# Performance work log

Measured on AMD Instinct MI355X. Metric: run time of the kernel, lower is better.

The kernel has to match this reference:

```python
import jax, jax.numpy as jnp
import numpy as np

H, IN, L, R = 128, 64, 3, 7
Nc, Na, Nx = 10000, 40000, 100000
NS = (Nc, Na, Nx)
ES = (50000, 100000, 100000, 150000, 200000, 200000, 200000)
# relation order: cc, c->a, a->c, aa, a->x, x->a, xx  (0=core,1=agg,2=access)
SRC_T = (0, 0, 1, 1, 1, 2, 2)
DST_T = (0, 1, 0, 1, 2, 1, 2)


def setup_inputs() -> dict:
    key = jax.random.key(0)
    ks = iter(jax.random.split(key, 80))
    d = {}
    for name, n in (("x_core", Nc), ("x_agg", Na), ("x_access", Nx)):
        d[name] = jax.random.normal(next(ks), (n, IN), jnp.float32)
    for r in range(R):
        d[f"src{r}"] = jax.random.randint(next(ks), (ES[r],), 0, NS[SRC_T[r]])
        d[f"dst{r}"] = jax.random.randint(next(ks), (ES[r],), 0, NS[DST_T[r]])
        d[f"ea{r}"] = jax.random.normal(next(ks), (ES[r], 3), jnp.float32)

    def w(k, shape, fan):
        return (jax.random.normal(k, shape, jnp.float32) / np.float32(np.sqrt(fan)))

    for nt in ("core", "agg", "access"):
        d[f"linW_{nt}"] = w(next(ks), (IN, H), IN)
        d[f"linb_{nt}"] = jnp.zeros((H,), jnp.float32)
    d["eW"] = w(next(ks), (L, R, 3, H), 3)       # GINEConv edge Linear(3->H)
    d["eb"] = jnp.zeros((L, R, H), jnp.float32)
    d["W1"] = w(next(ks), (L, R, H, H), H)        # MLP first Linear
    d["b1"] = jnp.zeros((L, R, H), jnp.float32)
    d["g1"] = jnp.ones((L, R, H), jnp.float32)    # BatchNorm gamma
    d["be1"] = jnp.zeros((L, R, H), jnp.float32)  # BatchNorm beta
    d["W2"] = w(next(ks), (L, R, H, H), H)        # MLP second Linear
    d["b2"] = jnp.zeros((L, R, H), jnp.float32)
    return d


def _forward(x_core, x_agg, x_access,
             linW_core, linb_core, linW_agg, linb_agg, linW_access, linb_access,
             eW, eb, W1, b1, g1, be1, W2, b2, srcs, dsts, eas):
    elu = jax.nn.elu
    h = [elu(x_core @ linW_core + linb_core),
         elu(x_agg @ linW_agg + linb_agg),
         elu(x_access @ linW_access + linb_access)]
    bn_inv = 1.0 / jnp.sqrt(jnp.float32(1.0 + 1e-5))  # eval BN: running mean 0, var 1
    for l in range(L):
        out = [jnp.zeros_like(ht) for ht in h]
        for r in range(R):
            s, t = SRC_T[r], DST_T[r]
            # GINEConv message: ReLU(x_j + Lin(edge_attr))  -> [E, H]
            msg = jax.nn.relu(h[s][srcs[r]] + eas[r] @ eW[l, r] + eb[l, r])
            agg = jax.ops.segment_sum(msg, dsts[r], num_segments=h[t].shape[0])
            z = h[t] + agg  # (1+eps)*x_i + aggr, eps=0
            # PyG MLP([H,H,H]): Linear -> BatchNorm -> ReLU -> Linear
            z = jax.nn.relu((z @ W1[l, r] + b1[l, r]) * bn_inv * g1[l, r] + be1[l, r])
            out[t] = out[t] + (z @ W2[l, r] + b2[l, r])  # HeteroConv aggr='sum'
        # residual + ELU; dropout is identity in eval mode
        h = [elu(out[t] + h[t]) for t in range(3)]
    return tuple(h)


def reference(x_core, x_agg, x_access,
              src0, dst0, ea0, src1, dst1, ea1, src2, dst2, ea2,
              src3, dst3, ea3, src4, dst4, ea4, src5, dst5, ea5,
              src6, dst6, ea6,
              linW_core, linb_core, linW_agg, linb_agg, linW_access, linb_access,
              eW, eb, W1, b1, g1, be1, W2, b2):
    srcs = (src0, src1, src2, src3, src4, src5, src6)
    dsts = (dst0, dst1, dst2, dst3, dst4, dst5, dst6)
    eas = (ea0, ea1, ea2, ea3, ea4, ea5, ea6)
    return _forward(x_core, x_agg, x_access,
                    linW_core, linb_core, linW_agg, linb_agg, linW_access, linb_access,
                    eW, eb, W1, b1, g1, be1, W2, b2, srcs, dsts, eas)
```

## Files before the change

kernel.cpp:

```cpp
#include <hip/hip_runtime.h>
#include <math.h>

#define H 128

typedef __attribute__((ext_vector_type(8))) short short8;
typedef __attribute__((ext_vector_type(4))) float f32x4;

static const int SRC_T_[7] = {0, 0, 1, 1, 1, 2, 2};
static const int DST_T_[7] = {0, 1, 0, 1, 2, 1, 2};

__device__ __forceinline__ float eluf(float x) {
    return x > 0.f ? x : (__expf(x) - 1.f);
}
__device__ __forceinline__ unsigned short f2bf(float x) {
    union { float f; unsigned int u; } v; v.f = x;
    unsigned int r = v.u + 0x7fffu + ((v.u >> 16) & 1u);
    return (unsigned short)(r >> 16);
}
__device__ __forceinline__ float bf2f(unsigned int u) {
    union { unsigned int u; float f; } v; v.u = u << 16;
    return v.f;
}

#define GLDS16(gp, lp) __builtin_amdgcn_global_load_lds( \
    (const __attribute__((address_space(1))) void*)(gp), \
    (__attribute__((address_space(3))) void*)(lp), 16, 0, 0)

struct PreCtx {
    const int* dst[7];
    int* deg;
    int E[7], bOff[8], hOff[8];
    const float* W1; const float* W2; const float* linW[3];
    unsigned short* wp; unsigned short* wlin;
    int gEnd;
};

__global__ __launch_bounds__(256) void k_pre(PreCtx P)
{
    const int b = blockIdx.x;
    const int tid = threadIdx.x;

    if (b < P.hOff[7]) {
        int r = 0;
        while (b >= P.hOff[r + 1]) ++r;
        const int lb = b - P.hOff[r];
        const int nb = P.hOff[r + 1] - P.hOff[r];
        const int* dst = P.dst[r];
        int* degr = P.deg + (P.bOff[r] << 8);
        for (int e = lb * 256 + tid; e < P.E[r]; e += nb * 256)
            atomicAdd(&degr[dst[e]], 1);
        return;
    }
    {
        const int lb = b - P.hOff[7];
        const int gw = P.gEnd - P.hOff[7];
        for (int i = lb * 256 + tid; i < 21 * 16384; i += gw * 256) {
            int lr = i >> 14, rem = i & 16383;
            int c = rem >> 7, k = rem & 127;
            P.wp[(size_t)(lr * 2 + 0) * 16384 + rem] = f2bf(P.W1[(size_t)lr * 16384 + k * H + c]);
            P.wp[(size_t)(lr * 2 + 1) * 16384 + rem] = f2bf(P.W2[(size_t)lr * 16384 + k * H + c]);
        }
        for (int i = lb * 256 + tid; i < 3 * 8192; i += gw * 256) {
            int t = i >> 13, rem = i & 8191;
            int c = rem >> 6, k = rem & 63;
            P.wlin[t * 8192 + c * 64 + k] = f2bf(P.linW[t][k * H + c]);
        }
    }
}

struct InCtx {
    const float* x[3]; const float* linb[3];
    unsigned short* hb[3]; int n[3];
    int gend[3];
};

__global__ __launch_bounds__(512, 2) void k_input_mfma(
    InCtx I, const unsigned short* __restrict__ wlin)
{
    __shared__ unsigned short xb[128 * 64];
    __shared__ unsigned short ob[128 * H];

    const int b = blockIdx.x;
    const int t = (b >= I.gend[0] ? 1 : 0) + (b >= I.gend[1] ? 1 : 0);
    const int lb = b - (t == 0 ? 0 : I.gend[t - 1]);
    const int n = I.n[t];
    const int tid = threadIdx.x;
    const int lane = tid & 63;
    const int wave = tid >> 6;
    const int wr = wave >> 2;
    const int wc = wave & 3;
    const int l15 = lane & 15;
    const int lq  = lane >> 4;
    const int c0 = wc * 32 + l15;
    const int r0 = lb * 128;
    const int rows = min(128, n - r0);
    const float* x = I.x[t];

    for (int idx = tid; idx < 128 * 16; idx += 512) {
        const int row = idx >> 4, cg = (idx & 15) << 2;
        uint2 p;
        if (row < rows) {
            f32x4 v = *(const f32x4*)&x[(size_t)(r0 + row) * 64 + cg];
            p.x = (unsigned int)f2bf(v.x) | ((unsigned int)f2bf(v.y) << 16);
            p.y = (unsigned int)f2bf(v.z) | ((unsigned int)f2bf(v.w) << 16);
        } else { p.x = 0; p.y = 0; }
        *(uint2*)&xb[row * 64 + (cg ^ ((row & 7) << 3))] = p;
    }
    const unsigned short* wt = wlin + (size_t)t * 8192;
    short8 wf[2][2];
#pragma unroll
    for (int nf = 0; nf < 2; ++nf)
#pragma unroll
        for (int kc = 0; kc < 2; ++kc)
            wf[nf][kc] = *(const short8*)&wt[(c0 + nf * 16) * 64 + kc * 32 + (lq << 3)];
    const float bc0 = I.linb[t][c0], bc1 = I.linb[t][c0 + 16];
    __syncthreads();

    const f32x4 Z4 = {0.f, 0.f, 0.f, 0.f};
    f32x4 acc[4][2];
#pragma unroll
    for (int rb = 0; rb < 4; ++rb)
#pragma unroll
        for (int nf = 0; nf < 2; ++nf) acc[rb][nf] = Z4;
#pragma unroll
    for (int kc = 0; kc < 2; ++kc) {
        const int kb = kc * 32 + (lq << 3);
        short8 af[4];
#pragma unroll
        for (int rb = 0; rb < 4; ++rb) {
            const int row = wr * 64 + rb * 16 + l15;
            af[rb] = *(const short8*)&xb[row * 64 + (kb ^ ((row & 7) << 3))];
        }
#pragma unroll
        for (int rb = 0; rb < 4; ++rb)
#pragma unroll
            for (int nf = 0; nf < 2; ++nf)
                acc[rb][nf] = __builtin_amdgcn_mfma_f32_16x16x32_bf16(
                    af[rb], wf[nf][kc], acc[rb][nf], 0, 0, 0);
    }
#pragma unroll
    for (int rb = 0; rb < 4; ++rb)
#pragma unroll
        for (int nf = 0; nf < 2; ++nf) {
            const int col = c0 + nf * 16;
            const float bc = nf == 0 ? bc0 : bc1;
#pragma unroll
            for (int rg = 0; rg < 4; ++rg) {
                const int row = wr * 64 + rb * 16 + (lq << 2) + rg;
                ob[row * H + col] = f2bf(eluf(acc[rb][nf][rg] + bc));
            }
        }
    __syncthreads();
    uint2* d = (uint2*)&I.hb[t][(size_t)r0 * H];
    const uint2* s2 = (const uint2*)ob;
    for (int idx = tid; idx < rows * 32; idx += 512) d[idx] = s2[idx];
}

struct CsrCtx {
    const int* src[7]; const int* dst[7]; const float* ea[7];
    int* csr_src[7]; uint2* csr_ea[7]; int* ptr[7];
    int* deg; int* cursor; int* bsum;
    int eOff[8];
    int bOff[8];
    int nd[7];
};

__global__ __launch_bounds__(256) void k_scan_partial_all(CsrCtx C)
{
    __shared__ int s[256];
    const int b = blockIdx.x;
    int r = 0;
    while (b >= C.bOff[r + 1]) ++r;
    const int lb = b - C.bOff[r];
    const int tid = threadIdx.x;
    const int idx = lb * 256 + tid;
    s[tid] = idx < C.nd[r] ? C.deg[(C.bOff[r] << 8) + idx] : 0;
    __syncthreads();
    for (int off = 128; off > 0; off >>= 1) {
        if (tid < off) s[tid] += s[tid + off];
        __syncthreads();
    }
    if (tid == 0) C.bsum[b] = s[0];
}

__global__ __launch_bounds__(512) void k_scan_mid_all(CsrCtx C)
{
    __shared__ int s[512];
    const int r = blockIdx.x;
    const int nb = C.bOff[r + 1] - C.bOff[r];
    const int tid = threadIdx.x;
    const int v = tid < nb ? C.bsum[C.bOff[r] + tid] : 0;
    s[tid] = v;
    __syncthreads();
    for (int off = 1; off < 512; off <<= 1) {
        int t = (tid >= off) ? s[tid - off] : 0;
        __syncthreads();
        s[tid] += t;
        __syncthreads();
    }
    if (tid < nb) C.bsum[C.bOff[r] + tid] = s[tid] - v;
    if (tid == nb - 1) C.ptr[r][C.nd[r]] = s[tid];
}

__global__ __launch_bounds__(256) void k_scan_final_all(CsrCtx C)
{
    __shared__ int s[256];
    const int b = blockIdx.x;
    int r = 0;
    while (b >= C.bOff[r + 1]) ++r;
    const int lb = b - C.bOff[r];
    const int tid = threadIdx.x;
    const int idx = lb * 256 + tid;
    const int v = idx < C.nd[r] ? C.deg[(C.bOff[r] << 8) + idx] : 0;
    s[tid] = v;
    __syncthreads();
    for (int off = 1; off < 256; off <<= 1) {
        int t = (tid >= off) ? s[tid - off] : 0;
        __syncthreads();
        s[tid] += t;
        __syncthreads();
    }
    if (idx < C.nd[r]) {
        const int excl = s[tid] - v + C.bsum[b];
        C.ptr[r][idx] = excl;
        C.cursor[(C.bOff[r] << 8) + idx] = excl;
    }
}

__global__ __launch_bounds__(256) void k_scatter_all(CsrCtx C, int Etot)
{
    for (int e = blockIdx.x * 256 + threadIdx.x; e < Etot; e += gridDim.x * 256) {
        int r = 0;
        while (e >= C.eOff[r + 1]) ++r;
        const int le = e - C.eOff[r];
        const int d = C.dst[r][le];
        const int pos = atomicAdd(&C.cursor[(C.bOff[r] << 8) + d], 1);
        C.csr_src[r][pos] = C.src[r][le];
        const float* eap = C.ea[r] + (size_t)3 * le;
        uint2 p;
        p.x = (unsigned int)f2bf(eap[0]) | ((unsigned int)f2bf(eap[1]) << 16);
        p.y = (unsigned int)f2bf(eap[2]);
        C.csr_ea[r][pos] = p;
    }
}

struct AggCtx {
    const int* ptr[7]; const int* csr_src[7]; const uint2* csr_ea[7];
    const unsigned short* hsrc[7]; const unsigned short* hdst[7];
    unsigned short* z[7];
    int gOff[8];
    int nd[7];
};

__global__ __launch_bounds__(256) void k_aggz_all(
    AggCtx A, const float* __restrict__ eW, const float* __restrict__ eb, int l)
{
    const int b = blockIdx.x;
    int r = 0;
    while (b >= A.gOff[r + 1]) ++r;
    const int lb = b - A.gOff[r];
    const int wave = threadIdx.x >> 6;
    const int lane = threadIdx.x & 63;
    const int t2 = lane << 1;
    const int lr = l * 7 + r;
    const float* eWr = eW + (size_t)lr * 3 * H;
    const float* ebr = eb + (size_t)lr * H;
    const float w00 = eWr[t2],         w01 = eWr[t2 + 1];
    const float w10 = eWr[H + t2],     w11 = eWr[H + t2 + 1];
    const float w20 = eWr[2 * H + t2], w21 = eWr[2 * H + t2 + 1];
    const float b0 = ebr[t2], b1v = ebr[t2 + 1];

    const int nd = A.nd[r];
    const int d0 = lb * 64 + wave * 16;
    if (d0 >= nd) return;
    const int dend = min(d0 + 16, nd);
    const int* __restrict__ ptr = A.ptr[r];
    const int* __restrict__ cs = A.csr_src[r];
    const uint2* __restrict__ ce = A.csr_ea[r];
    const unsigned short* __restrict__ hs = A.hsrc[r];
    const unsigned short* __restrict__ hd = A.hdst[r];
    unsigned int* __restrict__ zp = (unsigned int*)A.z[r];

    int pA = ptr[d0];
    int pB = ptr[d0 + 1];
    unsigned int hdvC = ((const unsigned int*)&hd[(size_t)d0 * H])[lane];

    for (int d = d0; d < dend; ++d) {
        int pNext = 0; unsigned int hdvN = 0;
        if (d + 1 < dend) {
            pNext = ptr[d + 2];
            hdvN = ((const unsigned int*)&hd[(size_t)(d + 1) * H])[lane];
        }
        float acc0 = bf2f(hdvC & 0xffffu);
        float acc1 = bf2f(hdvC >> 16);
        int i = pA;
        const int p1 = pB;
        if (i + 1 < p1) {
            int s0 = cs[i], s1 = cs[i + 1];
            uint2 eC0 = ce[i], eC1 = ce[i + 1];
            unsigned int hvC0 = ((const unsigned int*)&hs[(size_t)s0 * H])[lane];
            unsigned int hvC1 = ((const unsigned int*)&hs[(size_t)s1 * H])[lane];
            for (;;) {
                const int jn = i + 2;
                const bool more = (jn + 1 < p1);
                uint2 eN0, eN1; unsigned int hvN0 = 0, hvN1 = 0;
                if (more) {
                    const int sN0 = cs[jn], sN1 = cs[jn + 1];
                    eN0 = ce[jn]; eN1 = ce[jn + 1];
                    hvN0 = ((const unsigned int*)&hs[(size_t)sN0 * H])[lane];
                    hvN1 = ((const unsigned int*)&hs[(size_t)sN1 * H])[lane];
                }
                const float a00 = bf2f(eC0.x & 0xffffu), a01 = bf2f(eC0.x >> 16), a02 = bf2f(eC0.y & 0xffffu);
                const float a10 = bf2f(eC1.x & 0xffffu), a11 = bf2f(eC1.x >> 16), a12 = bf2f(eC1.y & 0xffffu);
                acc0 += fmaxf(bf2f(hvC0 & 0xffffu) + a00 * w00 + a01 * w10 + a02 * w20 + b0, 0.f)
                      + fmaxf(bf2f(hvC1 & 0xffffu) + a10 * w00 + a11 * w10 + a12 * w20 + b0, 0.f);
                acc1 += fmaxf(bf2f(hvC0 >> 16) + a00 * w01 + a01 * w11 + a02 * w21 + b1v, 0.f)
                      + fmaxf(bf2f(hvC1 >> 16) + a10 * w01 + a11 * w11 + a12 * w21 + b1v, 0.f);
                i = jn;
                if (!more) break;
                eC0 = eN0; eC1 = eN1; hvC0 = hvN0; hvC1 = hvN1;
            }
        }
        if (i < p1) {
            const int s = cs[i];
            const uint2 ep = ce[i];
            const float a0 = bf2f(ep.x & 0xffffu);
            const float a1 = bf2f(ep.x >> 16);
            const float a2 = bf2f(ep.y & 0xffffu);
            const unsigned int hv = ((const unsigned int*)&hs[(size_t)s * H])[lane];
            acc0 += fmaxf(bf2f(hv & 0xffffu) + a0 * w00 + a1 * w10 + a2 * w20 + b0, 0.f);
            acc1 += fmaxf(bf2f(hv >> 16)     + a0 * w01 + a1 * w11 + a2 * w21 + b1v, 0.f);
        }
        zp[(size_t)d * 64 + (lane ^ ((d & 7) << 2))] =
            (unsigned int)f2bf(acc0) | ((unsigned int)f2bf(acc1) << 16);
        pA = pB; pB = pNext; hdvC = hdvN;
    }
}

struct MlpCtx {
    const unsigned short* z[3][3];
    int lr[3][3];
    int nrel[3];
    int gend[3];
    int noffH[3];
    int n[3];
};

__global__ __launch_bounds__(512, 2) void k_mlp_all(
    MlpCtx M, const unsigned short* __restrict__ hb,
    unsigned short* __restrict__ hbw, float* __restrict__ fout,
    const unsigned short* __restrict__ wprep,
    const float* __restrict__ b1g, const float* __restrict__ g1g,
    const float* __restrict__ be1g, const float* __restrict__ b2g, int fin)
{
    __shared__ unsigned short smem[2 * 128 * H];
    unsigned short* zt  = smem;
    unsigned short* a1t = smem + 128 * H;

    const int b = blockIdx.x;
    const int t = (b >= M.gend[0] ? 1 : 0) + (b >= M.gend[1] ? 1 : 0);
    const int lb = b - (t == 0 ? 0 : M.gend[t - 1]);
    const int n = M.n[t];
    const int nrel = M.nrel[t];
    const unsigned short* hbp = hb + (size_t)M.noffH[t];

    const int tid = threadIdx.x;
    const int lane = tid & 63;
    const int wave = tid >> 6;
    const int wr = wave >> 2;
    const int wc = wave & 3;
    const int l15 = lane & 15;
    const int lq  = lane >> 4;
    const int c0 = wc * 32 + l15;

    const int r0 = lb * 128;
    const int rows = min(128, n - r0);
    const bool full = (rows == 128);

    auto stage = [&](const unsigned short* z) {
        const unsigned short* zsrc = z + (size_t)r0 * H;
        if (full) {
#pragma unroll
            for (int it = 0; it < 4; ++it) {
                const int off = (wave * 4 + it) * 512;
                GLDS16(zsrc + off + lane * 8, zt + off);
            }
        } else {
            for (int idx = tid; idx < rows * 16; idx += 512) {
                *(uint4*)&zt[idx * 8] = *(const uint4*)&zsrc[idx * 8];
            }
        }
    };

    const float bn_inv = 0.99999500003749977f;
    const f32x4 Z4 = {0.f, 0.f, 0.f, 0.f};
    f32x4 acc2[4][2];
#pragma unroll
    for (int rb = 0; rb < 4; ++rb)
#pragma unroll
        for (int nf = 0; nf < 2; ++nf) acc2[rb][nf] = Z4;
    float b2s0 = 0.f, b2s1 = 0.f;

    stage(M.z[t][0]);

    for (int rl = 0; rl < nrel; ++rl) {
        const int lr = M.lr[t][rl];
        const unsigned short* wp = wprep + (size_t)lr * 32768;
        short8 w1f[2][4], w2f[2][4];
#pragma unroll
        for (int nf = 0; nf < 2; ++nf)
#pragma unroll
            for (int kc = 0; kc < 4; ++kc) {
                w1f[nf][kc] = *(const short8*)&wp[(c0 + nf * 16) * H + kc * 32 + (lq << 3)];
                w2f[nf][kc] = *(const short8*)&wp[16384 + (c0 + nf * 16) * H + kc * 32 + (lq << 3)];
            }
        const float b1c0 = b1g[lr * H + c0],            b1c1 = b1g[lr * H + c0 + 16];
        const float sc0  = g1g[lr * H + c0] * bn_inv,   sc1  = g1g[lr * H + c0 + 16] * bn_inv;
        const float be0  = be1g[lr * H + c0],           be1v = be1g[lr * H + c0 + 16];
        b2s0 += b2g[lr * H + c0]; b2s1 += b2g[lr * H + c0 + 16];

        __syncthreads();

        f32x4 acc1[4][2];
#pragma unroll
        for (int rb = 0; rb < 4; ++rb)
#pragma unroll
            for (int nf = 0; nf < 2; ++nf) acc1[rb][nf] = Z4;
#pragma unroll
        for (int kc = 0; kc < 4; ++kc) {
            const int kb = kc * 32 + (lq << 3);
            short8 af[4];
#pragma unroll
            for (int rb = 0; rb < 4; ++rb) {
                const int row = wr * 64 + rb * 16 + l15;
                af[rb] = *(const short8*)&zt[row * H + (kb ^ ((row & 7) << 3))];
            }
#pragma unroll
            for (int rb = 0; rb < 4; ++rb)
#pragma unroll
                for (int nf = 0; nf < 2; ++nf)
                    acc1[rb][nf] = __builtin_amdgcn_mfma_f32_16x16x32_bf16(
                        af[rb], w1f[nf][kc], acc1[rb][nf], 0, 0, 0);
        }
#pragma unroll
        for (int rb = 0; rb < 4; ++rb)
#pragma unroll
            for (int nf = 0; nf < 2; ++nf) {
                const int col = c0 + nf * 16;
                const float b1c = nf == 0 ? b1c0 : b1c1;
                const float scv = nf == 0 ? sc0 : sc1;
                const float bev = nf == 0 ? be0 : be1v;
#pragma unroll
                for (int rg = 0; rg < 4; ++rg) {
                    const int row = wr * 64 + rb * 16 + (lq << 2) + rg;
                    float v = fmaxf((acc1[rb][nf][rg] + b1c) * scv + bev, 0.f);
                    a1t[row * H + (col ^ ((row & 7) << 3))] = f2bf(v);
                }
            }
        __syncthreads();

        if (rl + 1 < nrel) stage(M.z[t][rl + 1]);

#pragma unroll
        for (int kc = 0; kc < 4; ++kc) {
            const int kb = kc * 32 + (lq << 3);
            short8 af[4];
#pragma unroll
            for (int rb = 0; rb < 4; ++rb) {
                const int row = wr * 64 + rb * 16 + l15;
                af[rb] = *(const short8*)&a1t[row * H + (kb ^ ((row & 7) << 3))];
            }
#pragma unroll
            for (int rb = 0; rb < 4; ++rb)
#pragma unroll
                for (int nf = 0; nf < 2; ++nf)
                    acc2[rb][nf] = __builtin_amdgcn_mfma_f32_16x16x32_bf16(
                        af[rb], w2f[nf][kc], acc2[rb][nf], 0, 0, 0);
        }
    }

    if (fin) {
        float* fb = (float*)smem;
        float* foutp = fout + (size_t)M.noffH[t];
        __syncthreads();
#pragma unroll
        for (int rb = 0; rb < 4; ++rb)
#pragma unroll
            for (int nf = 0; nf < 2; ++nf) {
                const int col = c0 + nf * 16;
                const float b2s = nf == 0 ? b2s0 : b2s1;
#pragma unroll
                for (int rg = 0; rg < 4; ++rg) {
                    const int row = wr * 64 + rb * 16 + (lq << 2) + rg;
                    if (row < rows) {
                        const size_t o = (size_t)(r0 + row) * H + col;
                        fb[row * H + col] = eluf(acc2[rb][nf][rg] + b2s
                                                 + bf2f((unsigned int)hbp[o]));
                    }
                }
            }
        __syncthreads();
        float4* d4 = (float4*)&foutp[(size_t)r0 * H];
        const float4* s4 = (const float4*)fb;
        for (int idx = tid; idx < rows * 32; idx += 512) d4[idx] = s4[idx];
    } else {
        unsigned short* hbwp = hbw + (size_t)M.noffH[t];
        __syncthreads();
#pragma unroll
        for (int rb = 0; rb < 4; ++rb)
#pragma unroll
            for (int nf = 0; nf < 2; ++nf) {
                const int col = c0 + nf * 16;
                const float b2s = nf == 0 ? b2s0 : b2s1;
#pragma unroll
                for (int rg = 0; rg < 4; ++rg) {
                    const int row = wr * 64 + rb * 16 + (lq << 2) + rg;
                    if (row < rows) {
                        const size_t o = (size_t)(r0 + row) * H + col;
                        a1t[row * H + col] = f2bf(eluf(acc2[rb][nf][rg] + b2s
                                                       + bf2f((unsigned int)hbp[o])));
                    }
                }
            }
        __syncthreads();
        uint2* d = (uint2*)&hbwp[(size_t)r0 * H];
        const uint2* s2 = (const uint2*)a1t;
        for (int idx = tid; idx < rows * 32; idx += 512) d[idx] = s2[idx];
    }
}

static inline int imin(int a, int b) { return a < b ? a : b; }
static inline int imax(int a, int b) { return a > b ? a : b; }
static inline size_t alignup(size_t x) { return (x + 255) & ~(size_t)255; }

extern "C" void kernel_launch(void* const* d_in, const int* in_sizes, int n_in,
                              void* d_out, int out_size, void* d_ws, size_t ws_size,
                              hipStream_t stream) {
    const float* xin[3] = {(const float*)d_in[0], (const float*)d_in[1], (const float*)d_in[2]};
    const int* src[7]; const int* dst[7]; const float* ea[7]; int E[7];
    for (int r = 0; r < 7; ++r) {
        src[r] = (const int*)d_in[3 + 3 * r];
        dst[r] = (const int*)d_in[4 + 3 * r];
        ea[r]  = (const float*)d_in[5 + 3 * r];
        E[r]   = in_sizes[3 + 3 * r];
    }
    const float* linW[3] = {(const float*)d_in[24], (const float*)d_in[26], (const float*)d_in[28]};
    const float* linb[3] = {(const float*)d_in[25], (const float*)d_in[27], (const float*)d_in[29]};
    const float* eW  = (const float*)d_in[30];
    const float* ebp = (const float*)d_in[31];
    const float* W1  = (const float*)d_in[32];
    const float* b1  = (const float*)d_in[33];
    const float* g1  = (const float*)d_in[34];
    const float* be1 = (const float*)d_in[35];
    const float* W2  = (const float*)d_in[36];
    const float* b2  = (const float*)d_in[37];

    const int NSn[3]  = {in_sizes[0] / 64, in_sizes[1] / 64, in_sizes[2] / 64};
    const int NTOT = NSn[0] + NSn[1] + NSn[2];
    const int noff[3] = {0, NSn[0], NSn[0] + NSn[1]};

    float* fout = (float*)d_out;

    int eOff[8]; eOff[0] = 0;
    for (int r = 0; r < 7; ++r) eOff[r + 1] = eOff[r] + E[r];
    const int Etot = eOff[7];
    int bOff[8]; bOff[0] = 0;
    for (int r = 0; r < 7; ++r) bOff[r + 1] = bOff[r] + (NSn[DST_T_[r]] + 255) / 256;
    int gOff[8]; gOff[0] = 0;
    for (int r = 0; r < 7; ++r) gOff[r + 1] = gOff[r] + (NSn[DST_T_[r]] + 63) / 64;

    char* wsb = (char*)d_ws;
    size_t off = 0;
    unsigned short* hb = (unsigned short*)(wsb + off); off = alignup(off + (size_t)NTOT * H * 2);
    unsigned short* zb[7];
    for (int r = 0; r < 7; ++r) {
        int nd = NSn[DST_T_[r]];
        zb[r] = (unsigned short*)(wsb + off); off = alignup(off + (size_t)nd * H * 2);
    }
    unsigned short* wprep = (unsigned short*)(wsb + off); off = alignup(off + (size_t)21 * 32768 * 2);
    unsigned short* wlin  = (unsigned short*)(wsb + off); off = alignup(off + (size_t)3 * 8192 * 2);
    int* deg    = (int*)(wsb + off); off = alignup(off + (size_t)bOff[7] * 256 * 4);
    int* cursor = (int*)(wsb + off); off = alignup(off + (size_t)bOff[7] * 256 * 4);
    int* bsum   = (int*)(wsb + off); off = alignup(off + (size_t)bOff[7] * 4 + 256);
    int* ptrs[7]; int* csrs[7]; uint2* ceas[7];
    for (int r = 0; r < 7; ++r) {
        int nd = NSn[DST_T_[r]];
        ptrs[r] = (int*)(wsb + off); off = alignup(off + (size_t)(nd + 1) * 4);
    }
    for (int r = 0; r < 7; ++r) {
        csrs[r] = (int*)(wsb + off); off = alignup(off + (size_t)E[r] * 4);
    }
    for (int r = 0; r < 7; ++r) {
        ceas[r] = (uint2*)(wsb + off); off = alignup(off + (size_t)E[r] * 8);
    }

    PreCtx P;
    for (int r = 0; r < 7; ++r) { P.dst[r] = dst[r]; P.E[r] = E[r]; }
    P.deg = deg;
    for (int r = 0; r < 8; ++r) P.bOff[r] = bOff[r];
    P.hOff[0] = 0;
    for (int r = 0; r < 7; ++r)
        P.hOff[r + 1] = P.hOff[r] + imax(1, (E[r] + 1023) / 1024);
    P.W1 = W1; P.W2 = W2; P.wp = wprep; P.wlin = wlin;
    for (int t = 0; t < 3; ++t) P.linW[t] = linW[t];
    P.gEnd = P.hOff[7] + 256;

    hipMemsetAsync(deg, 0, (size_t)bOff[7] * 256 * 4, stream);
    k_pre<<<P.gEnd, 256, 0, stream>>>(P);

    InCtx I;
    int ig = 0;
    for (int t = 0; t < 3; ++t) {
        I.x[t] = xin[t]; I.linb[t] = linb[t];
        I.hb[t] = hb + (size_t)noff[t] * H; I.n[t] = NSn[t];
        ig += (NSn[t] + 127) / 128;
        I.gend[t] = ig;
    }
    k_input_mfma<<<ig, 512, 0, stream>>>(I, wlin);

    CsrCtx C;
    for (int r = 0; r < 7; ++r) {
        C.src[r] = src[r]; C.dst[r] = dst[r]; C.ea[r] = ea[r];
        C.csr_src[r] = csrs[r]; C.csr_ea[r] = ceas[r]; C.ptr[r] = ptrs[r];
        C.nd[r] = NSn[DST_T_[r]];
    }
    C.deg = deg; C.cursor = cursor; C.bsum = bsum;
    for (int r = 0; r < 8; ++r) { C.eOff[r] = eOff[r]; C.bOff[r] = bOff[r]; }

    k_scan_partial_all<<<bOff[7], 256, 0, stream>>>(C);
    k_scan_mid_all<<<7, 512, 0, stream>>>(C);
    k_scan_final_all<<<bOff[7], 256, 0, stream>>>(C);
    k_scatter_all<<<imin((Etot + 255) / 256, 8192), 256, 0, stream>>>(C, Etot);

    AggCtx A;
    for (int r = 0; r < 7; ++r) {
        A.ptr[r] = ptrs[r]; A.csr_src[r] = csrs[r]; A.csr_ea[r] = ceas[r];
        A.hsrc[r] = hb + (size_t)noff[SRC_T_[r]] * H;
        A.hdst[r] = hb + (size_t)noff[DST_T_[r]] * H;
        A.z[r] = zb[r];
        A.nd[r] = NSn[DST_T_[r]];
    }
    for (int r = 0; r < 8; ++r) A.gOff[r] = gOff[r];

    static const int RELS[3][3] = {{0, 2, 0}, {1, 3, 5}, {4, 6, 0}};
    static const int NRELS[3] = {2, 3, 2};
    MlpCtx M;
    int gend = 0;
    for (int t = 0; t < 3; ++t) {
        M.nrel[t] = NRELS[t];
        M.noffH[t] = noff[t] * H;
        M.n[t] = NSn[t];
        gend += (NSn[t] + 127) / 128;
        M.gend[t] = gend;
        for (int k = 0; k < 3; ++k) M.z[t][k] = zb[RELS[t][k]];
    }

    for (int l = 0; l < 3; ++l) {
        const int fin = (l == 2) ? 1 : 0;
        k_aggz_all<<<gOff[7], 256, 0, stream>>>(A, eW, ebp, l);
        for (int t = 0; t < 3; ++t)
            for (int k = 0; k < 3; ++k) M.lr[t][k] = l * 7 + RELS[t][k];
        k_mlp_all<<<M.gend[2], 512, 0, stream>>>(
            M, hb, hb, fout, wprep, b1, g1, be1, b2, fin);
    }
}
```

Measured before the change: 760.8 us.

## Make MLP kernel persistent with per-type block budget and cross-tile z prefetch

Replaces the one-block-per-128-row-tile launch of the fused MLP kernel with a persistent grid of about 512 blocks, split across node types in proportion to their tile counts. Each block loops over its tiles, and in non-final layers it prefetches the next tile's first z slice into LDS during the second GEMM. This is meant to cut block launch and tail overhead and overlap loads with compute, at the cost of weights being reloaded per relation per tile and possible load imbalance.

```diff
diff --git a/kernel.cpp b/kernel.cpp
--- a/kernel.cpp
+++ b/kernel.cpp
@@ -341,7 +341,8 @@
     const unsigned short* z[3][3];
     int lr[3][3];
     int nrel[3];
-    int gend[3];
+    int pend[3];
+    int ntile[3];
     int noffH[3];
     int n[3];
 };
@@ -358,8 +359,11 @@
     unsigned short* a1t = smem + 128 * H;
 
     const int b = blockIdx.x;
-    const int t = (b >= M.gend[0] ? 1 : 0) + (b >= M.gend[1] ? 1 : 0);
-    const int lb = b - (t == 0 ? 0 : M.gend[t - 1]);
+    const int t = (b >= M.pend[0] ? 1 : 0) + (b >= M.pend[1] ? 1 : 0);
+    const int lb = b - (t == 0 ? 0 : M.pend[t - 1]);
+    const int nbt = M.pend[t] - (t == 0 ? 0 : M.pend[t - 1]);
+    const int ntl = M.ntile[t];
+    if (lb >= ntl) return;
     const int n = M.n[t];
     const int nrel = M.nrel[t];
     const unsigned short* hbp = hb + (size_t)M.noffH[t];
@@ -373,159 +377,169 @@
     const int lq  = lane >> 4;
     const int c0 = wc * 32 + l15;
 
-    const int r0 = lb * 128;
-    const int rows = min(128, n - r0);
-    const bool full = (rows == 128);
-
-    auto stage = [&](const unsigned short* z) {
-        const unsigned short* zsrc = z + (size_t)r0 * H;
-        if (full) {
+    const float bn_inv = 0.99999500003749977f;
+    const f32x4 Z4 = {0.f, 0.f, 0.f, 0.f};
+
+    auto stage = [&](const unsigned short* z, int row0, int nrows) {
+        const unsigned short* zsrc = z + (size_t)row0 * H;
+        if (nrows == 128) {
 #pragma unroll
             for (int it = 0; it < 4; ++it) {
                 const int off = (wave * 4 + it) * 512;
                 GLDS16(zsrc + off + lane * 8, zt + off);
             }
         } else {
-            for (int idx = tid; idx < rows * 16; idx += 512) {
+            for (int idx = tid; idx < nrows * 16; idx += 512) {
                 *(uint4*)&zt[idx * 8] = *(const uint4*)&zsrc[idx * 8];
             }
         }
     };
 
-    const float bn_inv = 0.99999500003749977f;
-    const f32x4 Z4 = {0.f, 0.f, 0.f, 0.f};
-    f32x4 acc2[4][2];
-#pragma unroll
-    for (int rb = 0; rb < 4; ++rb)
-#pragma unroll
-        for (int nf = 0; nf < 2; ++nf) acc2[rb][nf] = Z4;
-    float b2s0 = 0.f, b2s1 = 0.f;
-
-    stage(M.z[t][0]);
-
-    for (int rl = 0; rl < nrel; ++rl) {
-        const int lr = M.lr[t][rl];
-        const unsigned short* wp = wprep + (size_t)lr * 32768;
-        short8 w1f[2][4], w2f[2][4];
-#pragma unroll
-        for (int nf = 0; nf < 2; ++nf)
+    bool prefetched = false;
+    for (int tile = lb; tile < ntl; tile += nbt) {
+        const int r0 = tile * 128;
+        const int rows = min(128, n - r0);
+        if (!prefetched) stage(M.z[t][0], r0, rows);
+        prefetched = false;
+
+        f32x4 acc2[4][2];
+#pragma unroll
+        for (int rb = 0; rb < 4; ++rb)
+#pragma unroll
+            for (int nf = 0; nf < 2; ++nf) acc2[rb][nf] = Z4;
+        float b2s0 = 0.f, b2s1 = 0.f;
+
+        for (int rl = 0; rl < nrel; ++rl) {
+            const int lr = M.lr[t][rl];
+            const unsigned short* wp = wprep + (size_t)lr * 32768;
+            short8 w1f[2][4], w2f[2][4];
+#pragma unroll
+            for (int nf = 0; nf < 2; ++nf)
+#pragma unroll
+                for (int kc = 0; kc < 4; ++kc) {
+                    w1f[nf][kc] = *(const short8*)&wp[(c0 + nf * 16) * H + kc * 32 + (lq << 3)];
+                    w2f[nf][kc] = *(const short8*)&wp[16384 + (c0 + nf * 16) * H + kc * 32 + (lq << 3)];
+                }
+            const float b1c0 = b1g[lr * H + c0],            b1c1 = b1g[lr * H + c0 + 16];
+            const float sc0  = g1g[lr * H + c0] * bn_inv,   sc1  = g1g[lr * H + c0 + 16] * bn_inv;
+            const float be0  = be1g[lr * H + c0],           be1v = be1g[lr * H + c0 + 16];
+            b2s0 += b2g[lr * H + c0]; b2s1 += b2g[lr * H + c0 + 16];
+
+            __syncthreads();
+
+            f32x4 acc1[4][2];
+#pragma unroll
+            for (int rb = 0; rb < 4; ++rb)
+#pragma unroll
+                for (int nf = 0; nf < 2; ++nf) acc1[rb][nf] = Z4;
 #pragma unroll
             for (int kc = 0; kc < 4; ++kc) {
-                w1f[nf][kc] = *(const short8*)&wp[(c0 + nf * 16) * H + kc * 32 + (lq << 3)];
-                w2f[nf][kc] = *(const short8*)&wp[16384 + (c0 + nf * 16) * H + kc * 32 + (lq << 3)];
+                const int kb = kc * 32 + (lq << 3);
+                short8 af[4];
+#pragma unroll
+                for (int rb = 0; rb < 4; ++rb) {
+                    const int row = wr * 64 + rb * 16 + l15;
+                    af[rb] = *(const short8*)&zt[row * H + (kb ^ ((row & 7) << 3))];
+                }
+#pragma unroll
+                for (int rb = 0; rb < 4; ++rb)
+#pragma unroll
+                    for (int nf = 0; nf < 2; ++nf)
+                        acc1[rb][nf] = __builtin_amdgcn_mfma_f32_16x16x32_bf16(
+                            af[rb], w1f[nf][kc], acc1[rb][nf], 0, 0, 0);
             }
-        const float b1c0 = b1g[lr * H + c0],            b1c1 = b1g[lr * H + c0 + 16];
-        const float sc0  = g1g[lr * H + c0] * bn_inv,   sc1  = g1g[lr * H + c0 + 16] * bn_inv;
-        const float be0  = be1g[lr * H + c0],           be1v = be1g[lr * H + c0 + 16];
-        b2s0 += b2g[lr * H + c0]; b2s1 += b2g[lr * H + c0 + 16];
-
-        __syncthreads();
-
-        f32x4 acc1[4][2];
-#pragma unroll
-        for (int rb = 0; rb < 4; ++rb)
-#pragma unroll
-            for (int nf = 0; nf < 2; ++nf) acc1[rb][nf] = Z4;
-#pragma unroll
-        for (int kc = 0; kc < 4; ++kc) {
-            const int kb = kc * 32 + (lq << 3);
-            short8 af[4];
-#pragma unroll
-            for (int rb = 0; rb < 4; ++rb) {
-                const int row = wr * 64 + rb * 16 + l15;
-                af[rb] = *(const short8*)&zt[row * H + (kb ^ ((row & 7) << 3))];
-            }
 #pragma unroll
             for (int rb = 0; rb < 4; ++rb)
 #pragma unroll
-                for (int nf = 0; nf < 2; ++nf)
-                    acc1[rb][nf] = __builtin_amdgcn_mfma_f32_16x16x32_bf16(
-                        af[rb], w1f[nf][kc], acc1[rb][nf], 0, 0, 0);
-        }
-#pragma unroll
-        for (int rb = 0; rb < 4; ++rb)
-#pragma unroll
-            for (int nf = 0; nf < 2; ++nf) {
-                const int col = c0 + nf * 16;
-                const float b1c = nf == 0 ? b1c0 : b1c1;
-                const float scv = nf == 0 ? sc0 : sc1;
-                const float bev = nf == 0 ? be0 : be1v;
-#pragma unroll
-                for (int rg = 0; rg < 4; ++rg) {
-                    const int row = wr * 64 + rb * 16 + (lq << 2) + rg;
-                    float v = fmaxf((acc1[rb][nf][rg] + b1c) * scv + bev, 0.f);
-                    a1t[row * H + (col ^ ((row & 7) << 3))] = f2bf(v);
-                }
-            }
-        __syncthreads();
-
-        if (rl + 1 < nrel) stage(M.z[t][rl + 1]);
-
-#pragma unroll
-        for (int kc = 0; kc < 4; ++kc) {
-            const int kb = kc * 32 + (lq << 3);
-            short8 af[4];
-#pragma unroll
-            for (int rb = 0; rb < 4; ++rb) {
-                const int row = wr * 64 + rb * 16 + l15;
-                af[rb] = *(const short8*)&a1t[row * H + (kb ^ ((row & 7) << 3))];
-            }
-#pragma unroll
-            for (int rb = 0; rb < 4; ++rb)
-#pragma unroll
-                for (int nf = 0; nf < 2; ++nf)
-                    acc2[rb][nf] = __builtin_amdgcn_mfma_f32_16x16x32_bf16(
-                        af[rb], w2f[nf][kc], acc2[rb][nf], 0, 0, 0);
-        }
-    }
-
-    if (fin) {
-        float* fb = (float*)smem;
-        float* foutp = fout + (size_t)M.noffH[t];
-        __syncthreads();
-#pragma unroll
-        for (int rb = 0; rb < 4; ++rb)
-#pragma unroll
-            for (int nf = 0; nf < 2; ++nf) {
-                const int col = c0 + nf * 16;
-                const float b2s = nf == 0 ? b2s0 : b2s1;
-#pragma unroll
-                for (int rg = 0; rg < 4; ++rg) {
-                    const int row = wr * 64 + rb * 16 + (lq << 2) + rg;
-                    if (row < rows) {
-                        const size_t o = (size_t)(r0 + row) * H + col;
-                        fb[row * H + col] = eluf(acc2[rb][nf][rg] + b2s
-                                                 + bf2f((unsigned int)hbp[o]));
+                for (int nf = 0; nf < 2; ++nf) {
+                    const int col = c0 + nf * 16;
+                    const float b1c = nf == 0 ? b1c0 : b1c1;
+                    const float scv = nf == 0 ? sc0 : sc1;
+                    const float bev = nf == 0 ? be0 : be1v;
+#pragma unroll
+                    for (int rg = 0; rg < 4; ++rg) {
+                        const int row = wr * 64 + rb * 16 + (lq << 2) + rg;
+                        float v = fmaxf((acc1[rb][nf][rg] + b1c) * scv + bev, 0.f);
+                        a1t[row * H + (col ^ ((row & 7) << 3))] = f2bf(v);
                     }
                 }
+            __syncthreads();
+
+            if (rl + 1 < nrel) {
+                stage(M.z[t][rl + 1], r0, rows);
+            } else if (!fin && tile + nbt < ntl) {
+                const int r0n = (tile + nbt) * 128;
+                stage(M.z[t][0], r0n, min(128, n - r0n));
+                prefetched = true;
             }
-        __syncthreads();
-        float4* d4 = (float4*)&foutp[(size_t)r0 * H];
-        const float4* s4 = (const float4*)fb;
-        for (int idx = tid; idx < rows * 32; idx += 512) d4[idx] = s4[idx];
-    } else {
-        unsigned short* hbwp = hbw + (size_t)M.noffH[t];
-        __syncthreads();
-#pragma unroll
-        for (int rb = 0; rb < 4; ++rb)
-#pragma unroll
-            for (int nf = 0; nf < 2; ++nf) {
-                const int col = c0 + nf * 16;
-                const float b2s = nf == 0 ? b2s0 : b2s1;
-#pragma unroll
-                for (int rg = 0; rg < 4; ++rg) {
-                    const int row = wr * 64 + rb * 16 + (lq << 2) + rg;
-                    if (row < rows) {
-                        const size_t o = (size_t)(r0 + row) * H + col;
-                        a1t[row * H + col] = f2bf(eluf(acc2[rb][nf][rg] + b2s
-                                                       + bf2f((unsigned int)hbp[o])));
+
+#pragma unroll
+            for (int kc = 0; kc < 4; ++kc) {
+                const int kb = kc * 32 + (lq << 3);
+                short8 af[4];
+#pragma unroll
+                for (int rb = 0; rb < 4; ++rb) {
+                    const int row = wr * 64 + rb * 16 + l15;
+                    af[rb] = *(const short8*)&a1t[row * H + (kb ^ ((row & 7) << 3))];
+                }
+#pragma unroll
+                for (int rb = 0; rb < 4; ++rb)
+#pragma unroll
+                    for (int nf = 0; nf < 2; ++nf)
+                        acc2[rb][nf] = __builtin_amdgcn_mfma_f32_16x16x32_bf16(
+                            af[rb], w2f[nf][kc], acc2[rb][nf], 0, 0, 0);
+            }
+        }
+
+        if (fin) {
+            float* fb = (float*)smem;
+            float* foutp = fout + (size_t)M.noffH[t];
+            __syncthreads();
+#pragma unroll
+            for (int rb = 0; rb < 4; ++rb)
+#pragma unroll
+                for (int nf = 0; nf < 2; ++nf) {
+                    const int col = c0 + nf * 16;
+                    const float b2s = nf == 0 ? b2s0 : b2s1;
+#pragma unroll
+                    for (int rg = 0; rg < 4; ++rg) {
+                        const int row = wr * 64 + rb * 16 + (lq << 2) + rg;
+                        if (row < rows) {
+                            const size_t o = (size_t)(r0 + row) * H + col;
+                            fb[row * H + col] = eluf(acc2[rb][nf][rg] + b2s
+                                                     + bf2f((unsigned int)hbp[o]));
+                        }
                     }
                 }
-            }
-        __syncthreads();
-        uint2* d = (uint2*)&hbwp[(size_t)r0 * H];
-        const uint2* s2 = (const uint2*)a1t;
-        for (int idx = tid; idx < rows * 32; idx += 512) d[idx] = s2[idx];
+            __syncthreads();
+            float4* d4 = (float4*)&foutp[(size_t)r0 * H];
+            const float4* s4 = (const float4*)fb;
+            for (int idx = tid; idx < rows * 32; idx += 512) d4[idx] = s4[idx];
+            __syncthreads();
+        } else {
+            unsigned short* hbwp = hbw + (size_t)M.noffH[t];
+            __syncthreads();
+#pragma unroll
+            for (int rb = 0; rb < 4; ++rb)
+#pragma unroll
+                for (int nf = 0; nf < 2; ++nf) {
+                    const int col = c0 + nf * 16;
+                    const float b2s = nf == 0 ? b2s0 : b2s1;
+#pragma unroll
+                    for (int rg = 0; rg < 4; ++rg) {
+                        const int row = wr * 64 + rb * 16 + (lq << 2) + rg;
+                        if (row < rows) {
+                            const size_t o = (size_t)(r0 + row) * H + col;
+                            a1t[row * H + col] = f2bf(eluf(acc2[rb][nf][rg] + b2s
+                                                           + bf2f((unsigned int)hbp[o])));
+                        }
+                    }
+                }
+            __syncthreads();
+            uint2* d = (uint2*)&hbwp[(size_t)r0 * H];
+            const uint2* s2 = (const uint2*)a1t;
+            for (int idx = tid; idx < rows * 32; idx += 512) d[idx] = s2[idx];
+        }
     }
 }
 
@@ -645,13 +659,18 @@
     static const int RELS[3][3] = {{0, 2, 0}, {1, 3, 5}, {4, 6, 0}};
     static const int NRELS[3] = {2, 3, 2};
     MlpCtx M;
-    int gend = 0;
+    int tiles[3], ttot = 0;
+    for (int t = 0; t < 3; ++t) { tiles[t] = (NSn[t] + 127) / 128; ttot += tiles[t]; }
+    int pend = 0;
     for (int t = 0; t < 3; ++t) {
         M.nrel[t] = NRELS[t];
         M.noffH[t] = noff[t] * H;
         M.n[t] = NSn[t];
-        gend += (NSn[t] + 127) / 128;
-        M.gend[t] = gend;
+        M.ntile[t] = tiles[t];
+        int nb = imax(1, (int)((long long)512 * tiles[t] / ttot));
+        nb = imin(nb, tiles[t]);
+        pend += nb;
+        M.pend[t] = pend;
         for (int k = 0; k < 3; ++k) M.z[t][k] = zb[RELS[t][k]];
     }
 
@@ -660,7 +679,7 @@
         k_aggz_all<<<gOff[7], 256, 0, stream>>>(A, eW, ebp, l);
         for (int t = 0; t < 3; ++t)
             for (int k = 0; k < 3; ++k) M.lr[t][k] = l * 7 + RELS[t][k];
-        k_mlp_all<<<M.gend[2], 512, 0, stream>>>(
+        k_mlp_all<<<M.pend[2], 512, 0, stream>>>(
             M, hb, hb, fout, wprep, b1, g1, be1, b2, fin);
     }
 }
```

New measurement: 783.9 us. +3.0%, slower.
